# Performance work log

Measured on AMD Instinct MI355X. Metric: run time of the kernel, lower is better.

Reference implementation:

```python
import jax, jax.numpy as jnp
import numpy as np

AMOUNT = 0.02  # skimage random_noise(mode='s&p', amount=0.02), salt_vs_pepper=0.5


def setup_inputs() -> dict:
    key = jax.random.key(0)
    k1, k2 = jax.random.split(key)
    B, C, H, W = 64, 3, 512, 512
    noised_image = jax.random.uniform(k1, (B, C, H, W), dtype=jnp.float32)
    noise_u = jax.random.uniform(k2, (B, C, H, W), dtype=jnp.float32)
    return {"noised_image": noised_image, "noise_u": noise_u}


def reference(noised_image, noise_u):
    # salt & pepper: fraction AMOUNT of pixels flipped; half -> pepper (0.0), half -> salt (1.0)
    half = jnp.asarray(AMOUNT * 0.5, noised_image.dtype)
    full = jnp.asarray(AMOUNT, noised_image.dtype)
    out = jnp.where(
        noise_u < half,
        jnp.asarray(0.0, noised_image.dtype),
        jnp.where(noise_u < full, jnp.asarray(1.0, noised_image.dtype), noised_image),
    )
    return out
```

## Files before the change

### kernel.cpp

```cpp
#include <hip/hip_runtime.h>


#define HALF_T 0.01f
#define FULL_T 0.02f

__global__ __launch_bounds__(256) void saltpepper_kernel(
    const float4* __restrict__ img,
    const float4* __restrict__ u,
    float4* __restrict__ out,
    int n4)
{
    int idx = blockIdx.x * blockDim.x + threadIdx.x;
    int stride = gridDim.x * blockDim.x;
    for (int i = idx; i < n4; i += stride) {
        float4 iv = img[i];
        float4 uv = u[i];
        float4 ov;
        ov.x = (uv.x < HALF_T) ? 0.0f : (uv.x < FULL_T) ? 1.0f : iv.x;
        ov.y = (uv.y < HALF_T) ? 0.0f : (uv.y < FULL_T) ? 1.0f : iv.y;
        ov.z = (uv.z < HALF_T) ? 0.0f : (uv.z < FULL_T) ? 1.0f : iv.z;
        ov.w = (uv.w < HALF_T) ? 0.0f : (uv.w < FULL_T) ? 1.0f : iv.w;
        out[i] = ov;
    }
}

__global__ __launch_bounds__(256) void saltpepper_tail_kernel(
    const float* __restrict__ img,
    const float* __restrict__ u,
    float* __restrict__ out,
    int start, int n)
{
    int i = start + blockIdx.x * blockDim.x + threadIdx.x;
    if (i < n) {
        float uv = u[i];
        out[i] = (uv < HALF_T) ? 0.0f : (uv < FULL_T) ? 1.0f : img[i];
    }
}

extern "C" void kernel_launch(void* const* d_in, const int* in_sizes, int n_in,
                              void* d_out, int out_size, void* d_ws, size_t ws_size,
                              hipStream_t stream) {
    const float* img = (const float*)d_in[0];
    const float* u   = (const float*)d_in[1];
    float* out = (float*)d_out;
    int n = in_sizes[0];

    int n4 = n / 4;
    int tail_start = n4 * 4;

    const int block = 256;
    int grid = (n4 + block - 1) / block;
    const int max_grid = 256 * 16;
    if (grid > max_grid) grid = max_grid;

    if (n4 > 0) {
        saltpepper_kernel<<<grid, block, 0, stream>>>(
            (const float4*)img, (const float4*)u, (float4*)out, n4);
    }

    int tail = n - tail_start;
    if (tail > 0) {
        int tgrid = (tail + block - 1) / block;
        saltpepper_tail_kernel<<<tgrid, block, 0, stream>>>(
            img, u, out, tail_start, n);
    }
}
```

Measured before the change: 451.1 us.

## Replace grid-stride loop with unrolled 4-vector-per-thread blocks and nontemporal stores

Drops the capped grid-stride loop and launches one block per 1024 float4 chunks. Each thread issues four independent 16-byte loads from each input before computing, which keeps more memory requests in flight. Output is written with nontemporal stores so it does not pollute the cache. Leftover float4 and scalar tails go to separate small kernels, which adds extra launches when n is not a multiple of 4096.

Result: no change. 450.6 us (-0.1%).

```diff
diff --git a/kernel.cpp b/kernel.cpp
--- a/kernel.cpp
+++ b/kernel.cpp
@@ -4,27 +4,57 @@
 #define HALF_T 0.01f
 #define FULL_T 0.02f
 
-__global__ __launch_bounds__(256) void saltpepper_kernel(
-    const float4* __restrict__ img,
-    const float4* __restrict__ u,
-    float4* __restrict__ out,
-    int n4)
+typedef float floatx4 __attribute__((ext_vector_type(4)));
+
+__device__ __forceinline__ floatx4 sp_select(floatx4 uv, floatx4 iv) {
+    floatx4 ov;
+    ov.x = (uv.x < HALF_T) ? 0.0f : (uv.x < FULL_T) ? 1.0f : iv.x;
+    ov.y = (uv.y < HALF_T) ? 0.0f : (uv.y < FULL_T) ? 1.0f : iv.y;
+    ov.z = (uv.z < HALF_T) ? 0.0f : (uv.z < FULL_T) ? 1.0f : iv.z;
+    ov.w = (uv.w < HALF_T) ? 0.0f : (uv.w < FULL_T) ? 1.0f : iv.w;
+    return ov;
+}
+
+__global__ __launch_bounds__(256) void saltpepper_x4_kernel(
+    const floatx4* __restrict__ img,
+    const floatx4* __restrict__ u,
+    floatx4* __restrict__ out)
 {
-    int idx = blockIdx.x * blockDim.x + threadIdx.x;
-    int stride = gridDim.x * blockDim.x;
-    for (int i = idx; i < n4; i += stride) {
-        float4 iv = img[i];
-        float4 uv = u[i];
-        float4 ov;
-        ov.x = (uv.x < HALF_T) ? 0.0f : (uv.x < FULL_T) ? 1.0f : iv.x;
-        ov.y = (uv.y < HALF_T) ? 0.0f : (uv.y < FULL_T) ? 1.0f : iv.y;
-        ov.z = (uv.z < HALF_T) ? 0.0f : (uv.z < FULL_T) ? 1.0f : iv.z;
-        ov.w = (uv.w < HALF_T) ? 0.0f : (uv.w < FULL_T) ? 1.0f : iv.w;
-        out[i] = ov;
+    int base = blockIdx.x * 1024 + threadIdx.x;
+
+    floatx4 u0 = u[base];
+    floatx4 u1 = u[base + 256];
+    floatx4 u2 = u[base + 512];
+    floatx4 u3 = u[base + 768];
+    floatx4 i0 = img[base];
+    floatx4 i1 = img[base + 256];
+    floatx4 i2 = img[base + 512];
+    floatx4 i3 = img[base + 768];
+
+    floatx4 o0 = sp_select(u0, i0);
+    floatx4 o1 = sp_select(u1, i1);
+    floatx4 o2 = sp_select(u2, i2);
+    floatx4 o3 = sp_select(u3, i3);
+
+    __builtin_nontemporal_store(o0, &out[base]);
+    __builtin_nontemporal_store(o1, &out[base + 256]);
+    __builtin_nontemporal_store(o2, &out[base + 512]);
+    __builtin_nontemporal_store(o3, &out[base + 768]);
+}
+
+__global__ __launch_bounds__(256) void saltpepper_f4_tail_kernel(
+    const floatx4* __restrict__ img,
+    const floatx4* __restrict__ u,
+    floatx4* __restrict__ out,
+    int start4, int n4)
+{
+    int i = start4 + blockIdx.x * blockDim.x + threadIdx.x;
+    if (i < n4) {
+        out[i] = sp_select(u[i], img[i]);
     }
 }
 
-__global__ __launch_bounds__(256) void saltpepper_tail_kernel(
+__global__ __launch_bounds__(256) void saltpepper_scalar_tail_kernel(
     const float* __restrict__ img,
     const float* __restrict__ u,
     float* __restrict__ out,
@@ -46,22 +76,24 @@
     int n = in_sizes[0];
 
     int n4 = n / 4;
-    int tail_start = n4 * 4;
+    int nb = n4 / 1024;
+    int f4_done = nb * 1024;
+    int sc_done = n4 * 4;
 
-    const int block = 256;
-    int grid = (n4 + block - 1) / block;
-    const int max_grid = 256 * 16;
-    if (grid > max_grid) grid = max_grid;
-
-    if (n4 > 0) {
-        saltpepper_kernel<<<grid, block, 0, stream>>>(
-            (const float4*)img, (const float4*)u, (float4*)out, n4);
+    if (nb > 0) {
+        saltpepper_x4_kernel<<<nb, 256, 0, stream>>>(
+            (const floatx4*)img, (const floatx4*)u, (floatx4*)out);
     }
-
-    int tail = n - tail_start;
-    if (tail > 0) {
-        int tgrid = (tail + block - 1) / block;
-        saltpepper_tail_kernel<<<tgrid, block, 0, stream>>>(
-            img, u, out, tail_start, n);
+    int f4_tail = n4 - f4_done;
+    if (f4_tail > 0) {
+        int g = (f4_tail + 255) / 256;
+        saltpepper_f4_tail_kernel<<<g, 256, 0, stream>>>(
+            (const floatx4*)img, (const floatx4*)u, (floatx4*)out, f4_done, n4);
+    }
+    int sc_tail = n - sc_done;
+    if (sc_tail > 0) {
+        int g = (sc_tail + 255) / 256;
+        saltpepper_scalar_tail_kernel<<<g, 256, 0, stream>>>(
+            img, u, out, sc_done, n);
     }
 }
```
